# Kernel optimization log

Measured on AMD Instinct MI355X. Metric: run time of the kernel, lower is better.

The kernel has to match this reference:

```python
import jax, jax.numpy as jnp
import numpy as np
import math

DIM = 1024
N_HEADS = 16
HEAD_DIM = DIM // N_HEADS
MAX_SEQ_LEN = 2048


def rope_tables(seq_len, head_dim):
    inv_freq = 1.0 / (10000.0 ** (jnp.arange(0, head_dim, 2, dtype=jnp.float32) / head_dim))
    t = jnp.arange(seq_len, dtype=jnp.float32)
    freqs = jnp.einsum('i,j->ij', t, inv_freq)          # [T, D/2]
    emb = jnp.concatenate([freqs, freqs], axis=-1)      # [T, D]
    return jnp.cos(emb), jnp.sin(emb)


def rotate_half(x):
    x1, x2 = jnp.split(x, 2, axis=-1)
    return jnp.concatenate([-x2, x1], axis=-1)


def setup_inputs() -> dict:
    key = jax.random.key(0)
    k1, k2, k3 = jax.random.split(key, 3)
    B, T = 4, 2048
    x = jax.random.normal(k1, (B, T, DIM), dtype=jnp.float32)
    # Linear(dim, 3*dim, bias=False) and Linear(dim, dim, bias=False); stored as [in, out]
    Wqkv = jax.random.normal(k2, (DIM, 3 * DIM), dtype=jnp.float32) * (1.0 / math.sqrt(DIM))
    Wproj = jax.random.normal(k3, (DIM, DIM), dtype=jnp.float32) * (1.0 / math.sqrt(DIM))
    return {"x": x, "Wqkv": Wqkv, "Wproj": Wproj}


def reference(x, Wqkv, Wproj):
    B, T, C = x.shape
    qkv = x @ Wqkv                                       # [B,T,3C]
    q, k, v = jnp.split(qkv, 3, axis=-1)
    # [B,T,C] -> [B,H,T,D]
    def to_heads(t_):
        return t_.reshape(B, T, N_HEADS, HEAD_DIM).transpose(0, 2, 1, 3)
    q, k, v = to_heads(q), to_heads(k), to_heads(v)
    cos, sin = rope_tables(T, HEAD_DIM)                  # [T,D]
    cos = cos[None, None, :, :]
    sin = sin[None, None, :, :]
    q = q * cos + rotate_half(q) * sin
    k = k * cos + rotate_half(k) * sin
    scale = 1.0 / math.sqrt(HEAD_DIM)
    att = jnp.einsum('bhqd,bhkd->bhqk', q, k) * scale    # [B,H,T,T]
    causal = jnp.triu(jnp.ones((T, T), dtype=bool), k=1)
    att = jnp.where(causal[None, None], -jnp.inf, att)
    att = jax.nn.softmax(att, axis=-1)
    y = jnp.einsum('bhqk,bhkd->bhqd', att, v)            # [B,H,T,D]
    y = y.transpose(0, 2, 1, 3).reshape(B, T, C)
    return y @ Wproj
```

## Files before the change

kernel.cpp:

```cpp
#include <hip/hip_runtime.h>
#include <hip/hip_bf16.h>

typedef unsigned short u16;
typedef __attribute__((ext_vector_type(8))) short short8;
typedef __attribute__((ext_vector_type(4))) float floatx4;

__device__ __forceinline__ u16 f2bf(float f) {
    union { float f; unsigned u; } v; v.f = f;
    unsigned r = v.u + 0x7fffu + ((v.u >> 16) & 1u);
    return (u16)(r >> 16);
}
__device__ __forceinline__ float fexp2(float x) {
#if __has_builtin(__builtin_amdgcn_exp2f)
    return __builtin_amdgcn_exp2f(x);
#else
    return exp2f(x);
#endif
}
__device__ __forceinline__ unsigned cvtpk_bf16(float lo, float hi) {
    unsigned r;
    asm("v_cvt_pk_bf16_f32 %0, %1, %2" : "=v"(r) : "v"(lo), "v"(hi));
    return r;
}
__device__ __forceinline__ void permlane32_swap(unsigned &a, unsigned &b) {
    asm("v_permlane32_swap_b32 %0, %1" : "+v"(a), "+v"(b));
}
__device__ __forceinline__ void permlane16_swap(unsigned &a, unsigned &b) {
    asm("v_permlane16_swap_b32 %0, %1" : "+v"(a), "+v"(b));
}

__device__ __forceinline__ void async_load16(const void* g, void* l) {
    __builtin_amdgcn_global_load_lds(
        (const __attribute__((address_space(1))) unsigned int*)g,
        (__attribute__((address_space(3))) unsigned int*)l, 16, 0, 0);
}

#define B_   4
#define T_   2048
#define NH_  16
#define HD_  64
#define DIM_ 1024
#define M_   (B_ * T_)
#define NQKV (3 * DIM_)
#define NT_  16
#define LOG2E 1.4426950408889634f

__global__ __launch_bounds__(256) void preproc(const float* __restrict__ x,
                                               const float* __restrict__ Wqkv,
                                               const float* __restrict__ Wproj,
                                               u16* __restrict__ xb,
                                               u16* __restrict__ wqt,
                                               u16* __restrict__ wpt,
                                               float* __restrict__ tabc,
                                               float* __restrict__ tabs) {
    __shared__ float tile[32][33];
    const int bid = blockIdx.x, tid = threadIdx.x;
    if (bid < 8192) {
        int idx = bid * 256 + tid;
        float4 v = ((const float4*)x)[idx];
        ushort4 o;
        o.x = f2bf(v.x); o.y = f2bf(v.y); o.z = f2bf(v.z); o.w = f2bf(v.w);
        ((ushort4*)xb)[idx] = o;
    } else if (bid < 12288) {
        const float* in; u16* outp; int Cn, bx, by;
        if (bid < 11264) { int blk = bid - 8192;  in = Wqkv;  outp = wqt; Cn = NQKV; bx = blk % 96; by = blk / 96; }
        else             { int blk = bid - 11264; in = Wproj; outp = wpt; Cn = DIM_; bx = blk & 31; by = blk >> 5; }
        const int R = DIM_;
        int c0 = bx * 32, r0 = by * 32;
        int tx = tid & 31, ty = tid >> 5;
#pragma unroll
        for (int i = 0; i < 4; ++i)
            tile[ty + i * 8][tx] = in[(size_t)(r0 + ty + i * 8) * Cn + c0 + tx];
        __syncthreads();
#pragma unroll
        for (int i = 0; i < 4; ++i)
            outp[(size_t)(c0 + ty + i * 8) * R + r0 + tx] = f2bf(tile[tx][ty + i * 8]);
    } else {
        int idx = (bid - 12288) * 256 + tid;
        int t = idx >> 5, j = idx & 31;
        double invf = pow(10000.0, -(double)j / 32.0);
        double th = (double)t * invf;
        tabc[idx] = (float)cos(th);
        tabs[idx] = (float)sin(th);
    }
}

__device__ __forceinline__ void gemm_core(const u16* __restrict__ A,
                                          const u16* __restrict__ Bt,
                                          u16* smem, int m0, int n0, int tid,
                                          floatx4 (&acc)[4][4]) {
    const int wave = tid >> 6, lane = tid & 63;
    const int ln15 = lane & 15, quad = lane >> 4;
    const int wm = (wave & 1) * 64, wn = (wave >> 1) * 64;
    const int l8 = lane & 7, ld8 = lane >> 3;
    const int sgc = (l8 ^ ld8) * 8;
    const int K = DIM_;

    const u16* aS = A + (size_t)(m0 + wave * 16 + ld8) * K + sgc;
    const u16* bS = Bt + (size_t)(n0 + wave * 32 + ld8) * K + sgc;

    auto issueA_B0 = [&](int k2, u16* As2, u16* Bs2) {
        async_load16(aS + k2,          As2 + (wave * 16) * 64);
        async_load16(aS + 8 * K + k2,  As2 + (wave * 16 + 8) * 64);
        async_load16(bS + k2,          Bs2 + (wave * 32) * 64);
    };
    auto issueB123 = [&](int k2, u16* Bs2) {
        async_load16(bS + 8 * K + k2,  Bs2 + (wave * 32 + 8) * 64);
        async_load16(bS + 16 * K + k2, Bs2 + (wave * 32 + 16) * 64);
        async_load16(bS + 24 * K + k2, Bs2 + (wave * 32 + 24) * 64);
    };
    auto compute = [&](const u16* As_c, const u16* Bs_c, int c4) {
        short8 af[4], bfv[4];
#pragma unroll
        for (int i = 0; i < 4; ++i) {
            int row = wm + i * 16 + ln15;
            af[i] = *(const short8*)&As_c[row * 64 + (((c4 + quad) ^ (row & 7)) << 3)];
        }
#pragma unroll
        for (int j = 0; j < 4; ++j) {
            int row = wn + j * 16 + ln15;
            bfv[j] = *(const short8*)&Bs_c[row * 64 + (((c4 + quad) ^ (row & 7)) << 3)];
        }
        __builtin_amdgcn_s_setprio(1);
#pragma unroll
        for (int i = 0; i < 4; ++i)
#pragma unroll
            for (int j = 0; j < 4; ++j)
                acc[i][j] = __builtin_amdgcn_mfma_f32_16x16x32_bf16(
                    af[i], bfv[j], acc[i][j], 0, 0, 0);
        __builtin_amdgcn_s_setprio(0);
    };

    issueA_B0(0, smem, smem + 24576);
    issueB123(0, smem + 24576);
    issueA_B0(64, smem + 8192, smem + 24576 + 16384);
    issueB123(64, smem + 24576 + 16384);

#pragma unroll 1
    for (int t = 0; t < NT_; ++t) {
        if (t < NT_ - 1) asm volatile("s_waitcnt vmcnt(6)" ::: "memory");
        else             asm volatile("s_waitcnt vmcnt(0)" ::: "memory");
        __builtin_amdgcn_s_barrier();
        asm volatile("" ::: "memory");

        const int cb = t % 3, cb2 = (t + 2) % 3;
        const u16* As_c = smem + cb * 8192;
        const u16* Bs_c = smem + 24576 + cb * 16384;
        u16* As2 = smem + cb2 * 8192;
        u16* Bs2 = smem + 24576 + cb2 * 16384;
        const bool iss = t < NT_ - 2;
        const int k2 = (t + 2) * 64;

        if (iss) issueA_B0(k2, As2, Bs2);
        compute(As_c, Bs_c, 0);
        asm volatile("" ::: "memory");
        __builtin_amdgcn_s_barrier();
        asm volatile("" ::: "memory");

        if (iss) issueB123(k2, Bs2);
        compute(As_c, Bs_c, 4);
        asm volatile("" ::: "memory");
    }
}

__global__ __launch_bounds__(512, 2) void gemm_qkv(const u16* __restrict__ A,
                                                   const u16* __restrict__ Bt,
                                                   const float* __restrict__ tabc,
                                                   const float* __restrict__ tabs,
                                                   u16* __restrict__ Qo,
                                                   u16* __restrict__ Ko,
                                                   u16* __restrict__ Vt) {
    __shared__ __align__(16) u16 smem[73728];
    const int tid = threadIdx.x;
    const int bid = blockIdx.x;
    const int wg = (bid & 7) * 96 + (bid >> 3);
    const int bx = wg / 64, by = wg - bx * 64;
    const int m0 = by * 128, n0 = bx * 256;

    floatx4 acc[4][4] = {};
    gemm_core(A, Bt, smem, m0, n0, tid, acc);

    const int wave = tid >> 6, lane = tid & 63;
    const int ln15 = lane & 15, quad = lane >> 4;
    const int wm = (wave & 1) * 64, wn = (wave >> 1) * 64;

    __syncthreads();
    u16* Es = smem;
    const int sel = n0 >> 10;
    auto es_put = [&](int row, int col, u16 v) {
        int c = col >> 3;
        int pc = (c & 24) | ((c & 7) ^ (row & 7));
        Es[row * 256 + pc * 8 + (col & 7)] = v;
    };
    if (sel == 2) {
#pragma unroll
        for (int i = 0; i < 4; ++i)
#pragma unroll
            for (int j = 0; j < 4; ++j)
#pragma unroll
                for (int r = 0; r < 4; ++r)
                    es_put(wm + i * 16 + quad * 4 + r, wn + j * 16 + ln15,
                           f2bf(acc[i][j][r]));
    } else {
        const float scale = sel ? 1.0f : 0.125f * LOG2E;
#pragma unroll
        for (int i = 0; i < 4; ++i)
#pragma unroll
            for (int jjl = 0; jjl < 2; ++jjl) {
                int j = jjl * 16 + ln15;
#pragma unroll
                for (int r = 0; r < 4; ++r) {
                    int row = wm + i * 16 + quad * 4 + r;
                    int t = (m0 + row) & (T_ - 1);
                    float cs = tabc[t * 32 + j], sn = tabs[t * 32 + j];
                    float xl = acc[i][jjl][r], xh = acc[i][jjl + 2][r];
                    es_put(row, wn + j,      f2bf((xl * cs - xh * sn) * scale));
                    es_put(row, wn + j + 32, f2bf((xh * cs + xl * sn) * scale));
                }
            }
    }
    __syncthreads();
    if (sel == 2) {
        const int bq = m0 >> 11;
        const int t0 = m0 & (T_ - 1);
        const int h0 = (n0 & 1023) >> 6;
#pragma unroll
        for (int a = 0; a < 4; ++a) {
            int aid = tid + a * 512;
            int hh = aid >> 9;
            int rem = aid & 511;
            int tseg = rem >> 5;
            int d2 = rem & 31;
            int col = hh * 64 + 2 * d2;
            int cch = col >> 3;
            u16 lo8[8], hi8[8];
#pragma unroll
            for (int j = 0; j < 8; ++j) {
                int row = tseg * 8 + j;
                int pc = (cch & 24) | ((cch & 7) ^ (row & 7));
                unsigned w = *(const unsigned*)&Es[row * 256 + pc * 8 + (col & 7)];
                lo8[j] = (u16)(w & 0xffffu);
                hi8[j] = (u16)(w >> 16);
            }
            size_t ob = ((size_t)((bq * NH_ + h0 + hh) * HD_) + 2 * d2) * T_ + t0 + tseg * 8;
            *(uint4*)(Vt + ob) = *(const uint4*)lo8;
            *(uint4*)(Vt + ob + T_) = *(const uint4*)hi8;
        }
    } else {
        const int bb = m0 >> 11;
        u16* outqk = (sel == 1) ? Ko : Qo;
#pragma unroll
        for (int k = 0; k < 8; ++k) {
            int cid = tid + k * 512;
            int row = cid >> 5, c = cid & 31;
            int pc = (c & 24) | ((c & 7) ^ (row & 7));
            uint4 v = *(const uint4*)&Es[row * 256 + pc * 8];
            int h = ((n0 & 1023) >> 6) + (c >> 3);
            int d = (c & 7) * 8;
            int t = (m0 + row) & (T_ - 1);
            *(uint4*)&outqk[((size_t)(bb * NH_ + h) * T_ + t) * HD_ + d] = v;
        }
    }
}

__device__ __forceinline__ void gemm_core128(const u16* __restrict__ A,
                                             const u16* __restrict__ Bt,
                                             u16* smem, int m0, int n0, int tid,
                                             floatx4 (&acc)[4][4]) {
    const int wave = tid >> 6, lane = tid & 63;
    const int ln15 = lane & 15, quad = lane >> 4;
    const int wm = (wave & 1) * 64, wn = (wave >> 1) * 64;
    const int l8 = lane & 7, ld8 = lane >> 3;
    const int sgc = (l8 ^ ld8) * 8;
    const int K = DIM_;

    const u16* aS = A + (size_t)(m0 + wave * 32 + ld8) * K + sgc;
    const u16* bS = Bt + (size_t)(n0 + wave * 32 + ld8) * K + sgc;

    auto stage = [&](int k0, u16* buf) {
#pragma unroll
        for (int it = 0; it < 4; ++it) {
            async_load16(aS + (size_t)(it * 8) * K + k0,
                         buf + (wave * 32 + it * 8) * 64);
            async_load16(bS + (size_t)(it * 8) * K + k0,
                         buf + 8192 + (wave * 32 + it * 8) * 64);
        }
    };
    auto compute = [&](const u16* buf, int c4) {
        short8 af[4], bfv[4];
#pragma unroll
        for (int i = 0; i < 4; ++i) {
            int row = wm + i * 16 + ln15;
            af[i] = *(const short8*)&buf[row * 64 + (((c4 + quad) ^ (row & 7)) << 3)];
        }
#pragma unroll
        for (int j = 0; j < 4; ++j) {
            int row = wn + j * 16 + ln15;
            bfv[j] = *(const short8*)&buf[8192 + row * 64 + (((c4 + quad) ^ (row & 7)) << 3)];
        }
        __builtin_amdgcn_s_setprio(1);
#pragma unroll
        for (int i = 0; i < 4; ++i)
#pragma unroll
            for (int j = 0; j < 4; ++j)
                acc[i][j] = __builtin_amdgcn_mfma_f32_16x16x32_bf16(
                    af[i], bfv[j], acc[i][j], 0, 0, 0);
        __builtin_amdgcn_s_setprio(0);
    };

    stage(0, smem);
#pragma unroll 1
    for (int t = 0; t < NT_; ++t) {
        asm volatile("s_waitcnt vmcnt(0)" ::: "memory");
        __builtin_amdgcn_s_barrier();
        asm volatile("" ::: "memory");
        if (t + 1 < NT_) stage((t + 1) * 64, smem + ((t + 1) & 1) * 16384);
        const u16* cur = smem + (t & 1) * 16384;
        compute(cur, 0);
        compute(cur, 4);
        asm volatile("" ::: "memory");
    }
}

__global__ __launch_bounds__(256, 4) void gemm_proj(const u16* __restrict__ A,
                                                    const u16* __restrict__ Bt,
                                                    float* __restrict__ C) {
    __shared__ __align__(16) u16 smem[32768];
    const int tid = threadIdx.x;
    const int bid = blockIdx.x;
    const int local = bid >> 3;
    const int by = (bid & 7) * 8 + (local & 7);
    const int bx = local >> 3;
    const int m0 = by * 128, n0 = bx * 128;

    floatx4 acc[4][4] = {};
    gemm_core128(A, Bt, smem, m0, n0, tid, acc);

    const int wave = tid >> 6, lane = tid & 63;
    const int ln15 = lane & 15, quad = lane >> 4;
    const int wm = (wave & 1) * 64, wn = (wave >> 1) * 64;
#pragma unroll
    for (int i = 0; i < 4; ++i)
#pragma unroll
        for (int jj = 0; jj < 4; ++jj)
#pragma unroll
            for (int r = 0; r < 4; ++r) {
                int m = m0 + wm + i * 16 + quad * 4 + r;
                int n = n0 + wn + jj * 16 + ln15;
                C[(size_t)m * DIM_ + n] = acc[i][jj][r];
            }
}

__global__ __launch_bounds__(256, 5) void attn_kernel(const u16* __restrict__ Q,
                                                      const u16* __restrict__ Kh,
                                                      const u16* __restrict__ Vt,
                                                      u16* __restrict__ Y) {
    __shared__ __align__(16) u16 Kl[2][64 * 64];
    __shared__ __align__(16) u16 Vl[2][64 * 64];
    const int tid = threadIdx.x, wave = tid >> 6, lane = tid & 63;
    const int ln15 = lane & 15, quad = lane >> 4;
    const int bid = blockIdx.x;
    const int wg = (bid & 7) * 128 + (bid >> 3);
    const int p = wg & 15;
    const int bh = wg >> 4;
    const int b = bh >> 4, h = bh & 15;
    const int l8 = lane & 7, ld8 = lane >> 3;
    const int sgc = l8 ^ ld8;

    const u16* kbase = Kh + (size_t)bh * T_ * HD_;
    const u16* vbase = Vt + (size_t)bh * HD_ * T_;
    const short8 ones = {0x3F80, 0x3F80, 0x3F80, 0x3F80,
                         0x3F80, 0x3F80, 0x3F80, 0x3F80};
    const int srow = wave * 16;

#pragma unroll
    for (int half = 0; half < 2; ++half) {
        const int tidx = half ? p : (31 - p);
        const int q0 = tidx * 64;
        const int bm = q0 + srow;

        const u16* qp = Q + ((size_t)bh * T_ + bm + ln15) * HD_;
        short8 qf0 = *(const short8*)(qp + quad * 8);
        short8 qf1 = *(const short8*)(qp + 32 + quad * 8);

        floatx4 o[5] = {};

        __syncthreads();
#pragma unroll
        for (int it = 0; it < 2; ++it) {
            int r = srow + it * 8;
            async_load16(kbase + (size_t)(r + ld8) * HD_ + sgc * 8, &Kl[0][r * 64]);
            async_load16(vbase + (size_t)(r + ld8) * T_ + sgc * 8, &Vl[0][r * 64]);
        }

        for (int kt = 0; kt <= tidx; ++kt) {
            const int cur = kt & 1;
            __syncthreads();
            if (kt < tidx) {
                const int kn = (kt + 1) * 64;
#pragma unroll
                for (int it = 0; it < 2; ++it) {
                    int r = srow + it * 8;
                    async_load16(kbase + (size_t)(kn + r + ld8) * HD_ + sgc * 8,
                                 &Kl[cur ^ 1][r * 64]);
                    async_load16(vbase + (size_t)(r + ld8) * T_ + kn + sgc * 8,
                                 &Vl[cur ^ 1][r * 64]);
                }
            }
            floatx4 s[4] = {};
            __builtin_amdgcn_s_setprio(1);
#pragma unroll
            for (int nt = 0; nt < 4; ++nt) {
                int row = nt * 16 + ln15;
                short8 kf0 = *(const short8*)&Kl[cur][row * 64 + ((quad ^ (row & 7)) << 3)];
                short8 kf1 = *(const short8*)&Kl[cur][row * 64 + (((4 + quad) ^ (row & 7)) << 3)];
                s[nt] = __builtin_amdgcn_mfma_f32_16x16x32_bf16(kf0, qf0, s[nt], 0, 0, 0);
                s[nt] = __builtin_amdgcn_mfma_f32_16x16x32_bf16(kf1, qf1, s[nt], 0, 0, 0);
            }
            __builtin_amdgcn_s_setprio(0);
            if (kt == tidx) {
                const int lim = srow + ln15;
#pragma unroll
                for (int nt = 0; nt < 4; ++nt) {
                    int key = nt * 16 + quad * 4;
#pragma unroll
                    for (int r = 0; r < 4; ++r)
                        s[nt][r] = (key + r > lim) ? 0.f : fexp2(s[nt][r]);
                }
            } else {
#pragma unroll
                for (int nt = 0; nt < 4; ++nt)
#pragma unroll
                    for (int r = 0; r < 4; ++r) s[nt][r] = fexp2(s[nt][r]);
            }
            unsigned x0 = cvtpk_bf16(s[0][0], s[0][1]);
            unsigned x1 = cvtpk_bf16(s[1][0], s[1][1]);
            unsigned y0 = cvtpk_bf16(s[0][2], s[0][3]);
            unsigned y1 = cvtpk_bf16(s[1][2], s[1][3]);
            unsigned x2 = cvtpk_bf16(s[2][0], s[2][1]);
            unsigned x3 = cvtpk_bf16(s[3][0], s[3][1]);
            unsigned y2 = cvtpk_bf16(s[2][2], s[2][3]);
            unsigned y3 = cvtpk_bf16(s[3][2], s[3][3]);
            permlane32_swap(x0, x1); permlane16_swap(x0, x1);
            permlane32_swap(y0, y1); permlane16_swap(y0, y1);
            permlane32_swap(x2, x3); permlane16_swap(x2, x3);
            permlane32_swap(y2, y3); permlane16_swap(y2, y3);
            union { unsigned u[4]; short8 s8; } pk0, pk1;
            pk0.u[0] = x0; pk0.u[1] = y0; pk0.u[2] = x1; pk0.u[3] = y1;
            pk1.u[0] = x2; pk1.u[1] = y2; pk1.u[2] = x3; pk1.u[3] = y3;
            __builtin_amdgcn_s_setprio(1);
#pragma unroll
            for (int nt = 0; nt < 4; ++nt) {
                int row = nt * 16 + ln15;
                short8 vf0 = *(const short8*)&Vl[cur][row * 64 + ((quad ^ (row & 7)) << 3)];
                short8 vf1 = *(const short8*)&Vl[cur][row * 64 + (((4 + quad) ^ (row & 7)) << 3)];
                o[nt] = __builtin_amdgcn_mfma_f32_16x16x32_bf16(pk0.s8, vf0, o[nt], 0, 0, 0);
                o[nt] = __builtin_amdgcn_mfma_f32_16x16x32_bf16(pk1.s8, vf1, o[nt], 0, 0, 0);
            }
            o[4] = __builtin_amdgcn_mfma_f32_16x16x32_bf16(pk0.s8, ones, o[4], 0, 0, 0);
            o[4] = __builtin_amdgcn_mfma_f32_16x16x32_bf16(pk1.s8, ones, o[4], 0, 0, 0);
            __builtin_amdgcn_s_setprio(0);
        }
#pragma unroll
        for (int r = 0; r < 4; ++r) {
            float inv = 1.f / o[4][r];
            int row = bm + quad * 4 + r;
            u16* yp = Y + ((size_t)(b * T_ + row)) * DIM_ + h * HD_;
#pragma unroll
            for (int nt = 0; nt < 4; ++nt)
                yp[nt * 16 + ln15] = f2bf(o[nt][r] * inv);
        }
    }
}

extern "C" void kernel_launch(void* const* d_in, const int* in_sizes, int n_in,
                              void* d_out, int out_size, void* d_ws, size_t ws_size,
                              hipStream_t stream) {
    const float* x     = (const float*)d_in[0];
    const float* Wqkv  = (const float*)d_in[1];
    const float* Wproj = (const float*)d_in[2];
    float* out = (float*)d_out;
    char* ws = (char*)d_ws;

    const size_t SZ_XB  = (size_t)M_ * DIM_ * 2;
    const size_t SZ_WQT = (size_t)NQKV * DIM_ * 2;
    const size_t SZ_WPT = (size_t)DIM_ * DIM_ * 2;
    const size_t SZ_Q   = SZ_XB;
    const size_t SZ_TAB = (size_t)T_ * 32 * 4;

    u16*   xb   = (u16*)(ws);
    u16*   wqt  = (u16*)(ws + SZ_XB);
    u16*   wpt  = (u16*)(ws + SZ_XB + SZ_WQT);
    u16*   qb   = (u16*)(ws + SZ_XB + SZ_WQT + SZ_WPT);
    u16*   kb   = (u16*)(ws + SZ_XB + SZ_WQT + SZ_WPT + SZ_Q);
    u16*   vtb  = (u16*)(ws + SZ_XB + SZ_WQT + SZ_WPT + 3 * SZ_Q);
    float* tabc = (float*)(ws + SZ_XB + SZ_WQT + SZ_WPT + 4 * SZ_Q);
    float* tabs = (float*)(ws + SZ_XB + SZ_WQT + SZ_WPT + 4 * SZ_Q + SZ_TAB);
    u16*   yb   = xb;

    preproc<<<12544, 256, 0, stream>>>(x, Wqkv, Wproj, xb, wqt, wpt, tabc, tabs);
    gemm_qkv<<<768, 512, 0, stream>>>(xb, wqt, tabc, tabs, qb, kb, vtb);
    attn_kernel<<<1024, 256, 0, stream>>>(qb, kb, vtb, yb);
    gemm_proj<<<512, 256, 0, stream>>>(yb, wpt, out);
}
```

Measured before the change: 232.7 us.

## Double query tile per attention block to reuse K/V tiles across 32 rows per wave

Each attention workgroup now handles 128 query rows (32 per wave, as two 16-row MFMA sub-tiles) instead of 64. Every K/V tile staged in LDS is therefore used by twice as many query rows, and the grid is halved to 512 blocks. This cuts global and LDS traffic for K/V per unit of work and gives more MFMA work between barriers. In exchange it raises register pressure (launch bounds drop from 5 to 4), leaves fewer blocks for load balancing, and wastes more masked work on the diagonal tiles.

```diff
diff --git a/kernel.cpp b/kernel.cpp
--- a/kernel.cpp
+++ b/kernel.cpp
@@ -351,7 +351,7 @@
             }
 }
 
-__global__ __launch_bounds__(256, 5) void attn_kernel(const u16* __restrict__ Q,
+__global__ __launch_bounds__(256, 4) void attn_kernel(const u16* __restrict__ Q,
                                                       const u16* __restrict__ Kh,
                                                       const u16* __restrict__ Vt,
                                                       u16* __restrict__ Y) {
@@ -360,9 +360,9 @@
     const int tid = threadIdx.x, wave = tid >> 6, lane = tid & 63;
     const int ln15 = lane & 15, quad = lane >> 4;
     const int bid = blockIdx.x;
-    const int wg = (bid & 7) * 128 + (bid >> 3);
-    const int p = wg & 15;
-    const int bh = wg >> 4;
+    const int wg = (bid & 7) * 64 + (bid >> 3);
+    const int p = wg & 7;
+    const int bh = wg >> 3;
     const int b = bh >> 4, h = bh & 15;
     const int l8 = lane & 7, ld8 = lane >> 3;
     const int sgc = l8 ^ ld8;
@@ -375,15 +375,18 @@
 
 #pragma unroll
     for (int half = 0; half < 2; ++half) {
-        const int tidx = half ? p : (31 - p);
-        const int q0 = tidx * 64;
-        const int bm = q0 + srow;
-
-        const u16* qp = Q + ((size_t)bh * T_ + bm + ln15) * HD_;
-        short8 qf0 = *(const short8*)(qp + quad * 8);
-        short8 qf1 = *(const short8*)(qp + 32 + quad * 8);
-
-        floatx4 o[5] = {};
+        const int tidx = half ? p : (15 - p);
+        const int q0 = tidx * 128;
+        const int base_row = q0 + wave * 32;
+
+        const u16* qp0 = Q + ((size_t)bh * T_ + base_row + ln15) * HD_;
+        const u16* qp1 = qp0 + 16 * HD_;
+        short8 qf00 = *(const short8*)(qp0 + quad * 8);
+        short8 qf01 = *(const short8*)(qp0 + 32 + quad * 8);
+        short8 qf10 = *(const short8*)(qp1 + quad * 8);
+        short8 qf11 = *(const short8*)(qp1 + 32 + quad * 8);
+
+        floatx4 o0[5] = {}, o1[5] = {};
 
         __syncthreads();
 #pragma unroll
@@ -393,10 +396,11 @@
             async_load16(vbase + (size_t)(r + ld8) * T_ + sgc * 8, &Vl[0][r * 64]);
         }
 
-        for (int kt = 0; kt <= tidx; ++kt) {
+        const int NKT = 2 * tidx + 1;
+        for (int kt = 0; kt <= NKT; ++kt) {
             const int cur = kt & 1;
             __syncthreads();
-            if (kt < tidx) {
+            if (kt < NKT) {
                 const int kn = (kt + 1) * 64;
 #pragma unroll
                 for (int it = 0; it < 2; ++it) {
@@ -407,68 +411,103 @@
                                  &Vl[cur ^ 1][r * 64]);
                 }
             }
-            floatx4 s[4] = {};
+            floatx4 s0[4] = {}, s1[4] = {};
             __builtin_amdgcn_s_setprio(1);
 #pragma unroll
             for (int nt = 0; nt < 4; ++nt) {
                 int row = nt * 16 + ln15;
                 short8 kf0 = *(const short8*)&Kl[cur][row * 64 + ((quad ^ (row & 7)) << 3)];
                 short8 kf1 = *(const short8*)&Kl[cur][row * 64 + (((4 + quad) ^ (row & 7)) << 3)];
-                s[nt] = __builtin_amdgcn_mfma_f32_16x16x32_bf16(kf0, qf0, s[nt], 0, 0, 0);
-                s[nt] = __builtin_amdgcn_mfma_f32_16x16x32_bf16(kf1, qf1, s[nt], 0, 0, 0);
+                s0[nt] = __builtin_amdgcn_mfma_f32_16x16x32_bf16(kf0, qf00, s0[nt], 0, 0, 0);
+                s0[nt] = __builtin_amdgcn_mfma_f32_16x16x32_bf16(kf1, qf01, s0[nt], 0, 0, 0);
+                s1[nt] = __builtin_amdgcn_mfma_f32_16x16x32_bf16(kf0, qf10, s1[nt], 0, 0, 0);
+                s1[nt] = __builtin_amdgcn_mfma_f32_16x16x32_bf16(kf1, qf11, s1[nt], 0, 0, 0);
             }
             __builtin_amdgcn_s_setprio(0);
-            if (kt == tidx) {
-                const int lim = srow + ln15;
+            if (kt >= 2 * tidx) {
+                const int koff = (kt - 2 * tidx) * 64;
+                const int lim0 = wave * 32 + ln15;
 #pragma unroll
                 for (int nt = 0; nt < 4; ++nt) {
-                    int key = nt * 16 + quad * 4;
-#pragma unroll
-                    for (int r = 0; r < 4; ++r)
-                        s[nt][r] = (key + r > lim) ? 0.f : fexp2(s[nt][r]);
+                    int key = koff + nt * 16 + quad * 4;
+#pragma unroll
+                    for (int r = 0; r < 4; ++r) {
+                        s0[nt][r] = (key + r > lim0) ? 0.f : fexp2(s0[nt][r]);
+                        s1[nt][r] = (key + r > lim0 + 16) ? 0.f : fexp2(s1[nt][r]);
+                    }
                 }
             } else {
 #pragma unroll
                 for (int nt = 0; nt < 4; ++nt)
 #pragma unroll
-                    for (int r = 0; r < 4; ++r) s[nt][r] = fexp2(s[nt][r]);
-            }
-            unsigned x0 = cvtpk_bf16(s[0][0], s[0][1]);
-            unsigned x1 = cvtpk_bf16(s[1][0], s[1][1]);
-            unsigned y0 = cvtpk_bf16(s[0][2], s[0][3]);
-            unsigned y1 = cvtpk_bf16(s[1][2], s[1][3]);
-            unsigned x2 = cvtpk_bf16(s[2][0], s[2][1]);
-            unsigned x3 = cvtpk_bf16(s[3][0], s[3][1]);
-            unsigned y2 = cvtpk_bf16(s[2][2], s[2][3]);
-            unsigned y3 = cvtpk_bf16(s[3][2], s[3][3]);
-            permlane32_swap(x0, x1); permlane16_swap(x0, x1);
-            permlane32_swap(y0, y1); permlane16_swap(y0, y1);
-            permlane32_swap(x2, x3); permlane16_swap(x2, x3);
-            permlane32_swap(y2, y3); permlane16_swap(y2, y3);
-            union { unsigned u[4]; short8 s8; } pk0, pk1;
-            pk0.u[0] = x0; pk0.u[1] = y0; pk0.u[2] = x1; pk0.u[3] = y1;
-            pk1.u[0] = x2; pk1.u[1] = y2; pk1.u[2] = x3; pk1.u[3] = y3;
+                    for (int r = 0; r < 4; ++r) {
+                        s0[nt][r] = fexp2(s0[nt][r]);
+                        s1[nt][r] = fexp2(s1[nt][r]);
+                    }
+            }
+            union { unsigned u[4]; short8 s8; } pa0, pb0, pa1, pb1;
+            {
+                unsigned x0 = cvtpk_bf16(s0[0][0], s0[0][1]);
+                unsigned x1 = cvtpk_bf16(s0[1][0], s0[1][1]);
+                unsigned y0 = cvtpk_bf16(s0[0][2], s0[0][3]);
+                unsigned y1 = cvtpk_bf16(s0[1][2], s0[1][3]);
+                unsigned x2 = cvtpk_bf16(s0[2][0], s0[2][1]);
+                unsigned x3 = cvtpk_bf16(s0[3][0], s0[3][1]);
+                unsigned y2 = cvtpk_bf16(s0[2][2], s0[2][3]);
+                unsigned y3 = cvtpk_bf16(s0[3][2], s0[3][3]);
+                permlane32_swap(x0, x1); permlane16_swap(x0, x1);
+                permlane32_swap(y0, y1); permlane16_swap(y0, y1);
+                permlane32_swap(x2, x3); permlane16_swap(x2, x3);
+                permlane32_swap(y2, y3); permlane16_swap(y2, y3);
+                pa0.u[0] = x0; pa0.u[1] = y0; pa0.u[2] = x1; pa0.u[3] = y1;
+                pb0.u[0] = x2; pb0.u[1] = y2; pb0.u[2] = x3; pb0.u[3] = y3;
+            }
+            {
+                unsigned x0 = cvtpk_bf16(s1[0][0], s1[0][1]);
+                unsigned x1 = cvtpk_bf16(s1[1][0], s1[1][1]);
+                unsigned y0 = cvtpk_bf16(s1[0][2], s1[0][3]);
+                unsigned y1 = cvtpk_bf16(s1[1][2], s1[1][3]);
+                unsigned x2 = cvtpk_bf16(s1[2][0], s1[2][1]);
+                unsigned x3 = cvtpk_bf16(s1[3][0], s1[3][1]);
+                unsigned y2 = cvtpk_bf16(s1[2][2], s1[2][3]);
+                unsigned y3 = cvtpk_bf16(s1[3][2], s1[3][3]);
+                permlane32_swap(x0, x1); permlane16_swap(x0, x1);
+                permlane32_swap(y0, y1); permlane16_swap(y0, y1);
+                permlane32_swap(x2, x3); permlane16_swap(x2, x3);
+                permlane32_swap(y2, y3); permlane16_swap(y2, y3);
+                pa1.u[0] = x0; pa1.u[1] = y0; pa1.u[2] = x1; pa1.u[3] = y1;
+                pb1.u[0] = x2; pb1.u[1] = y2; pb1.u[2] = x3; pb1.u[3] = y3;
+            }
             __builtin_amdgcn_s_setprio(1);
 #pragma unroll
             for (int nt = 0; nt < 4; ++nt) {
                 int row = nt * 16 + ln15;
                 short8 vf0 = *(const short8*)&Vl[cur][row * 64 + ((quad ^ (row & 7)) << 3)];
                 short8 vf1 = *(const short8*)&Vl[cur][row * 64 + (((4 + quad) ^ (row & 7)) << 3)];
-                o[nt] = __builtin_amdgcn_mfma_f32_16x16x32_bf16(pk0.s8, vf0, o[nt], 0, 0, 0);
-                o[nt] = __builtin_amdgcn_mfma_f32_16x16x32_bf16(pk1.s8, vf1, o[nt], 0, 0, 0);
-            }
-            o[4] = __builtin_amdgcn_mfma_f32_16x16x32_bf16(pk0.s8, ones, o[4], 0, 0, 0);
-            o[4] = __builtin_amdgcn_mfma_f32_16x16x32_bf16(pk1.s8, ones, o[4], 0, 0, 0);
+                o0[nt] = __builtin_amdgcn_mfma_f32_16x16x32_bf16(pa0.s8, vf0, o0[nt], 0, 0, 0);
+                o0[nt] = __builtin_amdgcn_mfma_f32_16x16x32_bf16(pb0.s8, vf1, o0[nt], 0, 0, 0);
+                o1[nt] = __builtin_amdgcn_mfma_f32_16x16x32_bf16(pa1.s8, vf0, o1[nt], 0, 0, 0);
+                o1[nt] = __builtin_amdgcn_mfma_f32_16x16x32_bf16(pb1.s8, vf1, o1[nt], 0, 0, 0);
+            }
+            o0[4] = __builtin_amdgcn_mfma_f32_16x16x32_bf16(pa0.s8, ones, o0[4], 0, 0, 0);
+            o0[4] = __builtin_amdgcn_mfma_f32_16x16x32_bf16(pb0.s8, ones, o0[4], 0, 0, 0);
+            o1[4] = __builtin_amdgcn_mfma_f32_16x16x32_bf16(pa1.s8, ones, o1[4], 0, 0, 0);
+            o1[4] = __builtin_amdgcn_mfma_f32_16x16x32_bf16(pb1.s8, ones, o1[4], 0, 0, 0);
             __builtin_amdgcn_s_setprio(0);
         }
 #pragma unroll
         for (int r = 0; r < 4; ++r) {
-            float inv = 1.f / o[4][r];
-            int row = bm + quad * 4 + r;
-            u16* yp = Y + ((size_t)(b * T_ + row)) * DIM_ + h * HD_;
+            float inv0 = 1.f / o0[4][r];
+            int row0 = base_row + quad * 4 + r;
+            u16* yp0 = Y + ((size_t)(b * T_ + row0)) * DIM_ + h * HD_;
 #pragma unroll
             for (int nt = 0; nt < 4; ++nt)
-                yp[nt * 16 + ln15] = f2bf(o[nt][r] * inv);
+                yp0[nt * 16 + ln15] = f2bf(o0[nt][r] * inv0);
+            float inv1 = 1.f / o1[4][r];
+            u16* yp1 = yp0 + (size_t)16 * DIM_;
+#pragma unroll
+            for (int nt = 0; nt < 4; ++nt)
+                yp1[nt * 16 + ln15] = f2bf(o1[nt][r] * inv1);
         }
     }
 }
@@ -500,6 +539,6 @@
 
     preproc<<<12544, 256, 0, stream>>>(x, Wqkv, Wproj, xb, wqt, wpt, tabc, tabs);
     gemm_qkv<<<768, 512, 0, stream>>>(xb, wqt, tabc, tabs, qb, kb, vtb);
-    attn_kernel<<<1024, 256, 0, stream>>>(qb, kb, vtb, yb);
+    attn_kernel<<<512, 256, 0, stream>>>(qb, kb, vtb, yb);
     gemm_proj<<<512, 256, 0, stream>>>(yb, wpt, out);
 }
```

New measurement: 245.7 us. 1.06x slower.
